# Kernel optimization log

Measured on AMD Instinct MI355X. Metric: run time of the kernel, lower is better.

The kernel has to match this reference:

```python
import jax, jax.numpy as jnp
import numpy as np

B, N, K = 8, 2048, 100  # graphs per batch, nodes per graph, diffpool clusters


def _bn(x, g, b, eps=1e-5):
    # BatchNorm1d in training mode over all B*N nodes (biased variance)
    m = x.mean(axis=(0, 1))
    v = x.var(axis=(0, 1))
    return (x - m) * jax.lax.rsqrt(v + eps) * g + b


def _norm_adj(A):
    # PyG gcn_norm: add remaining self-loops (fill=1), D^-1/2 (A+I) D^-1/2
    n = A.shape[-1]
    d = jnp.diagonal(A, axis1=-2, axis2=-1)
    A_hat = A + jnp.where(d == 0, 1.0, 0.0)[..., :, None] * jnp.eye(n, dtype=A.dtype)
    deg = A_hat.sum(-1)
    dinv = jnp.where(deg > 0, 1.0 / jnp.sqrt(deg), 0.0)
    return dinv[..., :, None] * A_hat * dinv[..., None, :]


def _gcn(An, x, W, b):
    # GCNConv: propagate(x @ W) + bias, with pre-normalized adjacency
    return An @ (x @ W) + b


def _forward(x, adj, W_in, W3030, Wp13, b30, b100, Wfc_pool, bfc_pool,
             W1, b1, W2, b2, gamma30, beta30, gamma100, beta100):
    A_w = _norm_adj(adj)                               # weighted (edge_attr) adjacency
    A_b = _norm_adj((adj > 0).astype(adj.dtype))       # pool convs ignore edge_attr
    # feature branch
    x11 = _bn(_gcn(A_w, x, W_in[0], b30[0]), gamma30[0], beta30[0])
    x12 = _bn(_gcn(A_w, x11, W3030[0], b30[1]), gamma30[1], beta30[1])
    x13 = _bn(_gcn(A_w, x12, W3030[1], b30[2]), gamma30[2], beta30[2])
    x1_out = jnp.concatenate([x11, x12, x13], -1).max(axis=1)   # [B,90]
    # assignment branch
    s11 = _bn(_gcn(A_b, x, W_in[1], b30[3]), gamma30[3], beta30[3])
    s12 = _bn(_gcn(A_b, s11, W3030[2], b30[4]), gamma30[4], beta30[4])
    s13 = _bn(_gcn(A_b, s12, Wp13, b100), gamma100, beta100)
    s1 = jnp.concatenate([s11, s12, s13], -1) @ Wfc_pool + bfc_pool  # [B,N,K]
    # dense_diff_pool (link/entropy losses are unused by the forward output)
    s = jax.nn.softmax(s1, -1)
    p1_x = jnp.einsum('bnk,bnd->bkd', s, x13)          # s^T x  [B,K,30]
    p1_adj = jnp.einsum('bnk,bnl->bkl', s, adj @ s)    # s^T A s  [B,K,K]
    # second stage on pooled (dense, weighted) graph
    A2 = _norm_adj(p1_adj)
    x21 = _bn(_gcn(A2, p1_x, W3030[3], b30[5]), gamma30[5], beta30[5])
    x22 = _bn(_gcn(A2, x21, W3030[4], b30[6]), gamma30[6], beta30[6])
    x23 = _bn(_gcn(A2, x22, W3030[5], b30[7]), gamma30[7], beta30[7])
    x2_out = jnp.concatenate([x21, x22, x23], -1).max(axis=1)   # [B,90]
    h = jnp.concatenate([x1_out, x2_out], -1) @ W1 + b1
    return jax.nn.relu(h) @ W2 + b2                    # [B,6]


def setup_inputs():
    key = jax.random.key(0)
    ks = jax.random.split(key, 12)
    u = jax.random.uniform(ks[0], (B, N, N), dtype=jnp.float32)
    mask = jax.random.uniform(ks[1], (B, N, N)) < 0.05
    A = jnp.triu(u * mask, 1)
    adj = A + jnp.swapaxes(A, -1, -2)
    x = jax.random.normal(ks[2], (B, N, 3), dtype=jnp.float32)
    w = lambda k, s: jax.random.normal(k, s, dtype=jnp.float32) * 0.1
    return dict(
        x=x, adj=adj,
        W_in=w(ks[3], (2, 3, 30)),      # conv11, pool_conv11
        W3030=w(ks[4], (6, 30, 30)),    # conv12, conv13, pool_conv12, conv21..23
        Wp13=w(ks[5], (30, 100)),
        b30=jnp.zeros((8, 30), jnp.float32),
        b100=jnp.zeros((100,), jnp.float32),
        Wfc_pool=w(ks[6], (160, 100)), bfc_pool=jnp.zeros((100,), jnp.float32),
        W1=w(ks[7], (180, 50)), b1=jnp.zeros((50,), jnp.float32),
        W2=w(ks[8], (50, 6)), b2=jnp.zeros((6,), jnp.float32),
        gamma30=jnp.ones((8, 30), jnp.float32), beta30=jnp.zeros((8, 30), jnp.float32),
        gamma100=jnp.ones((100,), jnp.float32), beta100=jnp.zeros((100,), jnp.float32),
    )


def reference(x, adj, W_in, W3030, Wp13, b30, b100, Wfc_pool, bfc_pool,
              W1, b1, W2, b2, gamma30, beta30, gamma100, beta100):
    return _forward(x, adj, W_in, W3030, Wp13, b30, b100, Wfc_pool, bfc_pool,
                    W1, b1, W2, b2, gamma30, beta30, gamma100, beta100)
```

## Files before the change

### kernel.cpp

```cpp
#include <hip/hip_runtime.h>
#include <hip/hip_fp16.h>
#include <cstdint>
#include <cstddef>

#define BATCH 8
#define NN 2048
#define RTOT 16384
#define CAP 176

static constexpr size_t OF_B1W   = 0;
static constexpr size_t OF_B1B   = 3840;
static constexpr size_t OF_B2W   = 7680;
static constexpr size_t OF_B2B   = 11520;
static constexpr size_t OF_B3W   = 15360;
static constexpr size_t OF_B3B   = 15840;
static constexpr size_t OF_S2    = 17440;
static constexpr size_t OF_CNT   = 17620;
static constexpr size_t ZEND     = 17632;
static constexpr size_t OF_ELLV  = 17664;
static constexpr size_t OF_ELLC  = OF_ELLV + 2883584;
static constexpr size_t OF_ROWLEN= OF_ELLC + 1441792;
static constexpr size_t OF_DINVW = OF_ROWLEN + 16384;
static constexpr size_t OF_DINVB = OF_DINVW + 16384;
static constexpr size_t OF_HWB   = OF_DINVB + 16384;
static constexpr size_t OF_HW3   = OF_HWB + 524288;
static constexpr size_t OF_HB100 = OF_HW3 + 262144;
static constexpr size_t OF_ZW    = OF_HB100 + 851968;
static constexpr size_t OF_ZB    = OF_ZW + 524288;
static constexpr size_t OF_X11   = OF_ZB + 1703936;
static constexpr size_t OF_X12   = OF_X11 + 524288;
static constexpr size_t OF_X13   = OF_X12 + 524288;
static constexpr size_t OF_S11   = OF_X13 + 524288;
static constexpr size_t OF_S12   = OF_S11 + 524288;
static constexpr size_t OF_PARTMAX = OF_S12 + 524288;
static constexpr size_t OF_PP    = OF_PARTMAX + 23040;
static constexpr size_t OF_PPOOL = OF_PP + 3328000;

#define FMA4(acc, s, h) { acc.x += (s)*(h).x; acc.y += (s)*(h).y; acc.z += (s)*(h).z; acc.w += (s)*(h).w; }

__device__ __forceinline__ unsigned short f2h(float f) {
  _Float16 h = (_Float16)f;
  return *(unsigned short*)&h;
}
__device__ __forceinline__ float h2f(unsigned short s) {
  _Float16 h = *(_Float16*)&s;
  return (float)h;
}
__device__ __forceinline__ float2 h2f2(unsigned int u) {
  __half2 h = *(__half2*)&u;
  return __half22float2(h);
}

struct __align__(8) us4 { unsigned short x, y, z, w; };

#define ACC8(g, wt) { \
  float2 f0=h2f2((g).x), f1=h2f2((g).y), f2=h2f2((g).z), f3=h2f2((g).w); \
  acc[0] += (wt)*f0.x; acc[1] += (wt)*f0.y; acc[2] += (wt)*f1.x; acc[3] += (wt)*f1.y; \
  acc[4] += (wt)*f2.x; acc[5] += (wt)*f2.y; acc[6] += (wt)*f3.x; acc[7] += (wt)*f3.y; }


__global__ __launch_bounds__(256) void k_build_ell(
    const float* __restrict__ adj, const float* __restrict__ x,
    const float* __restrict__ Win, float* __restrict__ ellv,
    unsigned short* __restrict__ ellc, int* __restrict__ rowlen,
    float* __restrict__ dinvw, float* __restrict__ dinvb,
    unsigned short* __restrict__ Hwb, float* __restrict__ zbase)
{
  int r = blockIdx.x;
  int t = threadIdx.x, lane = t & 63, wv = t >> 6;
  if (blockIdx.x < 69) {
    int zi = blockIdx.x * 256 + t;
    if (zi < (int)ZEND) zbase[zi] = 0.f;
  }
  const float* row = adj + (size_t)r * NN;
  __shared__ int wcnt[4];
  __shared__ float wsumA[4];
  __shared__ float dsh[2];
  float4 a = ((const float4*)row)[t];
  float4 b = ((const float4*)row)[256 + t];
  float vals[8] = {a.x, a.y, a.z, a.w, b.x, b.y, b.z, b.w};
  int cbase0 = t*4, cbase1 = 1024 + t*4;
  int cnt = 0; float sum = 0.f;
#pragma unroll
  for (int k = 0; k < 8; ++k) { sum += vals[k]; cnt += (vals[k] != 0.f) ? 1 : 0; }
  int pre = cnt;
#pragma unroll
  for (int o = 1; o < 64; o <<= 1) { int n = __shfl_up(pre, o); if (lane >= o) pre += n; }
  int excl = pre - cnt;
  int wtot = __shfl(pre, 63);
#pragma unroll
  for (int o = 32; o; o >>= 1) sum += __shfl_down(sum, o);
  if (lane == 0) { wcnt[wv] = wtot; wsumA[wv] = sum; }
  __syncthreads();
  int base = 0;
  for (int w = 0; w < wv; ++w) base += wcnt[w];
  int p = base + excl;
  size_t rb = (size_t)r * CAP;
#pragma unroll
  for (int k = 0; k < 8; ++k) {
    float v = vals[k];
    if (v != 0.f && p < CAP) {
      ellv[rb + p] = v;
      ellc[rb + p] = (unsigned short)((k < 4) ? (cbase0 + k) : (cbase1 + (k - 4)));
      ++p;
    }
  }
  if (t == 0) {
    int tot = wcnt[0] + wcnt[1] + wcnt[2] + wcnt[3];
    float ws = wsumA[0] + wsumA[1] + wsumA[2] + wsumA[3];
    int nnz = tot < CAP ? tot : CAP;
    int n = nnz;
    while ((n & 3) && n < CAP) { ellv[rb + n] = 0.f; ellc[rb + n] = 0; ++n; }
    rowlen[r] = n;
    float dw = rsqrtf(ws + 1.f), db = rsqrtf((float)nnz + 1.f);
    dinvw[r] = dw; dinvb[r] = db;
    dsh[0] = dw; dsh[1] = db;
  }
  __syncthreads();
  if (t < 64) {
    int c = t & 31, side = t >> 5;
    float v = 0.f;
    if (c < 30) {
      float x0 = x[r*3], x1 = x[r*3+1], x2 = x[r*3+2];
      const float* W = Win + side*90;
      v = (x0*W[c] + x1*W[30+c] + x2*W[60+c]) * dsh[side];
    }
    Hwb[(size_t)r*64 + t] = f2h(v);
  }
}

__global__ __launch_bounds__(256) void k_spmm_pair(
    const unsigned short* __restrict__ Hwb, const float* __restrict__ ellv,
    const unsigned short* __restrict__ ellc, const int* __restrict__ rowlen,
    const float* __restrict__ dinvw, const float* __restrict__ dinvb,
    float* __restrict__ Zw, float* __restrict__ Zb,
    float* __restrict__ bktW, float* __restrict__ bktB)
{
  __shared__ float zsW[32][32];
  __shared__ float zsB[32][32];
  int t = threadIdx.x;
  int gid = blockIdx.x * 256 + t;
  int row = gid >> 3, q = gid & 7;
  int side = q >> 2, sub = q & 3;
  int len = rowlen[row];
  const float4* ev = (const float4*)(ellv + (size_t)row * CAP);
  const uint2*  ec = (const uint2*) (ellc + (size_t)row * CAP);
  const uint4* HP = (const uint4*)(Hwb + (size_t)(row >> 11) * (NN*64));
  float acc[8] = {0,0,0,0,0,0,0,0};
  int nit = len >> 2;
  int i = 0;
  for (; i + 2 <= nit; i += 2) {
    float4 v0 = ev[i], v1 = ev[i+1];
    uint2 cc0 = ec[i], cc1 = ec[i+1];
    int a0 = cc0.x & 0xffff, a1 = cc0.x >> 16, a2 = cc0.y & 0xffff, a3 = cc0.y >> 16;
    int e0 = cc1.x & 0xffff, e1 = cc1.x >> 16, e2 = cc1.y & 0xffff, e3 = cc1.y >> 16;
    uint4 g0 = HP[a0*8+q], g1 = HP[a1*8+q], g2 = HP[a2*8+q], g3 = HP[a3*8+q];
    uint4 g4 = HP[e0*8+q], g5 = HP[e1*8+q], g6 = HP[e2*8+q], g7 = HP[e3*8+q];
    float w0 = side ? (v0.x>0.f?1.f:0.f) : v0.x;
    float w1 = side ? (v0.y>0.f?1.f:0.f) : v0.y;
    float w2 = side ? (v0.z>0.f?1.f:0.f) : v0.z;
    float w3 = side ? (v0.w>0.f?1.f:0.f) : v0.w;
    float w4 = side ? (v1.x>0.f?1.f:0.f) : v1.x;
    float w5 = side ? (v1.y>0.f?1.f:0.f) : v1.y;
    float w6 = side ? (v1.z>0.f?1.f:0.f) : v1.z;
    float w7 = side ? (v1.w>0.f?1.f:0.f) : v1.w;
    ACC8(g0, w0); ACC8(g1, w1); ACC8(g2, w2); ACC8(g3, w3);
    ACC8(g4, w4); ACC8(g5, w5); ACC8(g6, w6); ACC8(g7, w7);
  }
  if (i < nit) {
    float4 v = ev[i];
    uint2 cc = ec[i];
    int c0 = cc.x & 0xffff, c1 = cc.x >> 16, c2 = cc.y & 0xffff, c3 = cc.y >> 16;
    uint4 g0 = HP[c0*8+q], g1 = HP[c1*8+q], g2 = HP[c2*8+q], g3 = HP[c3*8+q];
    float w0 = side ? (v.x>0.f?1.f:0.f) : v.x;
    float w1 = side ? (v.y>0.f?1.f:0.f) : v.y;
    float w2 = side ? (v.z>0.f?1.f:0.f) : v.z;
    float w3 = side ? (v.w>0.f?1.f:0.f) : v.w;
    ACC8(g0, w0); ACC8(g1, w1); ACC8(g2, w2); ACC8(g3, w3);
  }
  uint4 hs = HP[(row & (NN-1))*8 + q];
  ACC8(hs, 1.f);
  float d = side ? dinvb[row] : dinvw[row];
#pragma unroll
  for (int k = 0; k < 8; ++k) acc[k] *= d;
  float* Zp = (side ? Zb : Zw) + (size_t)row*32 + sub*8;
  float4 o0 = {acc[0],acc[1],acc[2],acc[3]}, o1 = {acc[4],acc[5],acc[6],acc[7]};
  ((float4*)Zp)[0] = o0; ((float4*)Zp)[1] = o1;
  int rowloc = t >> 3;
  float (*zs)[32] = side ? zsB : zsW;
#pragma unroll
  for (int k = 0; k < 8; ++k) zs[rowloc][sub*8+k] = acc[k];
  __syncthreads();
  int copy = blockIdx.x & 63;
  if (t < 30) {
    float s1 = 0.f, s2 = 0.f;
    for (int r = 0; r < 32; ++r) { float v = zsW[r][t]; s1 += v; s2 += v*v; }
    atomicAdd(&bktW[(t*64+copy)*2],   s1);
    atomicAdd(&bktW[(t*64+copy)*2+1], s2);
  } else if (t >= 64 && t < 94) {
    int c = t - 64;
    float s1 = 0.f, s2 = 0.f;
    for (int r = 0; r < 32; ++r) { float v = zsB[r][c]; s1 += v; s2 += v*v; }
    atomicAdd(&bktB[(c*64+copy)*2],   s1);
    atomicAdd(&bktB[(c*64+copy)*2+1], s2);
  }
}

__global__ __launch_bounds__(256) void k_spmm_l3(
    const unsigned short* __restrict__ Hw3, const unsigned short* __restrict__ Hb100,
    const float* __restrict__ ellv, const unsigned short* __restrict__ ellc,
    const int* __restrict__ rowlen, const float* __restrict__ dinvw,
    const float* __restrict__ dinvb, float* __restrict__ Zw, float* __restrict__ Zb,
    float* __restrict__ bktW3, float* __restrict__ bktB3)
{
  __shared__ float zs[64][32];
  __shared__ float st[200];
  int t = threadIdx.x;
  if (blockIdx.x < 256) {
    int gid = blockIdx.x * 256 + t;
    int row = gid >> 2, q = gid & 3;
    int len = rowlen[row];
    const float4* ev = (const float4*)(ellv + (size_t)row * CAP);
    const uint2*  ec = (const uint2*) (ellc + (size_t)row * CAP);
    const uint4* HP = (const uint4*)(Hw3 + (size_t)(row >> 11) * (NN*32));
    float acc[8] = {0,0,0,0,0,0,0,0};
    int nit = len >> 2;
    int i = 0;
    for (; i + 2 <= nit; i += 2) {
      float4 v0 = ev[i], v1 = ev[i+1];
      uint2 cc0 = ec[i], cc1 = ec[i+1];
      int a0 = cc0.x & 0xffff, a1 = cc0.x >> 16, a2 = cc0.y & 0xffff, a3 = cc0.y >> 16;
      int e0 = cc1.x & 0xffff, e1 = cc1.x >> 16, e2 = cc1.y & 0xffff, e3 = cc1.y >> 16;
      uint4 g0 = HP[a0*4+q], g1 = HP[a1*4+q], g2 = HP[a2*4+q], g3 = HP[a3*4+q];
      uint4 g4 = HP[e0*4+q], g5 = HP[e1*4+q], g6 = HP[e2*4+q], g7 = HP[e3*4+q];
      ACC8(g0, v0.x); ACC8(g1, v0.y); ACC8(g2, v0.z); ACC8(g3, v0.w);
      ACC8(g4, v1.x); ACC8(g5, v1.y); ACC8(g6, v1.z); ACC8(g7, v1.w);
    }
    if (i < nit) {
      float4 v = ev[i];
      uint2 cc = ec[i];
      int c0 = cc.x & 0xffff, c1 = cc.x >> 16, c2 = cc.y & 0xffff, c3 = cc.y >> 16;
      uint4 g0 = HP[c0*4+q], g1 = HP[c1*4+q], g2 = HP[c2*4+q], g3 = HP[c3*4+q];
      ACC8(g0, v.x); ACC8(g1, v.y); ACC8(g2, v.z); ACC8(g3, v.w);
    }
    uint4 hs = HP[(row & (NN-1))*4 + q];
    ACC8(hs, 1.f);
    float d = dinvw[row];
#pragma unroll
    for (int k = 0; k < 8; ++k) acc[k] *= d;
    float* Zp = Zw + (size_t)row*32 + q*8;
    float4 o0 = {acc[0],acc[1],acc[2],acc[3]}, o1 = {acc[4],acc[5],acc[6],acc[7]};
    ((float4*)Zp)[0] = o0; ((float4*)Zp)[1] = o1;
    int rowloc = t >> 2;
#pragma unroll
    for (int k = 0; k < 8; ++k) zs[rowloc][q*8+k] = acc[k];
    __syncthreads();
    if (t < 30) {
      float s1 = 0.f, s2 = 0.f;
      for (int r = 0; r < 64; ++r) { float v = zs[r][t]; s1 += v; s2 += v*v; }
      int copy = blockIdx.x & 7;
      atomicAdd(&bktW3[(t*8+copy)*2],   s1);
      atomicAdd(&bktW3[(t*8+copy)*2+1], s2);
    }
  } else {
    int bid = blockIdx.x - 256;
    for (int i = t; i < 200; i += 256) st[i] = 0.f;
    __syncthreads();
    int gid = bid * 256 + t;
    int row = gid / 13, q = gid - row*13;
    int len = rowlen[row];
    const float4* ev = (const float4*)(ellv + (size_t)row * CAP);
    const uint2*  ec = (const uint2*) (ellc + (size_t)row * CAP);
    const uint4* HP = (const uint4*)(Hb100 + (size_t)(row >> 11) * ((size_t)NN*104));
    float acc[8] = {0,0,0,0,0,0,0,0};
    int nit = len >> 2;
    int i = 0;
    for (; i + 2 <= nit; i += 2) {
      float4 v0 = ev[i], v1 = ev[i+1];
      uint2 cc0 = ec[i], cc1 = ec[i+1];
      int a0 = cc0.x & 0xffff, a1 = cc0.x >> 16, a2 = cc0.y & 0xffff, a3 = cc0.y >> 16;
      int e0 = cc1.x & 0xffff, e1 = cc1.x >> 16, e2 = cc1.y & 0xffff, e3 = cc1.y >> 16;
      uint4 g0 = HP[a0*13+q], g1 = HP[a1*13+q], g2 = HP[a2*13+q], g3 = HP[a3*13+q];
      uint4 g4 = HP[e0*13+q], g5 = HP[e1*13+q], g6 = HP[e2*13+q], g7 = HP[e3*13+q];
      float w0 = (v0.x>0.f?1.f:0.f), w1 = (v0.y>0.f?1.f:0.f);
      float w2 = (v0.z>0.f?1.f:0.f), w3 = (v0.w>0.f?1.f:0.f);
      float w4 = (v1.x>0.f?1.f:0.f), w5 = (v1.y>0.f?1.f:0.f);
      float w6 = (v1.z>0.f?1.f:0.f), w7 = (v1.w>0.f?1.f:0.f);
      ACC8(g0, w0); ACC8(g1, w1); ACC8(g2, w2); ACC8(g3, w3);
      ACC8(g4, w4); ACC8(g5, w5); ACC8(g6, w6); ACC8(g7, w7);
    }
    if (i < nit) {
      float4 v = ev[i];
      uint2 cc = ec[i];
      int c0 = cc.x & 0xffff, c1 = cc.x >> 16, c2 = cc.y & 0xffff, c3 = cc.y >> 16;
      uint4 g0 = HP[c0*13+q], g1 = HP[c1*13+q], g2 = HP[c2*13+q], g3 = HP[c3*13+q];
      float w0 = (v.x>0.f?1.f:0.f), w1 = (v.y>0.f?1.f:0.f);
      float w2 = (v.z>0.f?1.f:0.f), w3 = (v.w>0.f?1.f:0.f);
      ACC8(g0, w0); ACC8(g1, w1); ACC8(g2, w2); ACC8(g3, w3);
    }
    uint4 hs = HP[(row & (NN-1))*13 + q];
    ACC8(hs, 1.f);
    float d = dinvb[row];
#pragma unroll
    for (int k = 0; k < 8; ++k) acc[k] *= d;
    float* Zp = Zb + (size_t)row*104 + q*8;
    float4 o0 = {acc[0],acc[1],acc[2],acc[3]}, o1 = {acc[4],acc[5],acc[6],acc[7]};
    ((float4*)Zp)[0] = o0; ((float4*)Zp)[1] = o1;
    int c0 = q*8;
#pragma unroll
    for (int k = 0; k < 8; ++k) {
      int ch = c0 + k;
      if (ch < 100) { atomicAdd(&st[ch*2], acc[k]); atomicAdd(&st[ch*2+1], acc[k]*acc[k]); }
    }
    __syncthreads();
    int copy = bid & 7;
    for (int i2 = t; i2 < 200; i2 += 256)
      atomicAdd(&bktB3[((i2>>1)*8 + copy)*2 + (i2&1)], st[i2]);
  }
}

template<int LEVEL>
__global__ __launch_bounds__(256) void k_apply_gemm(
    const float* __restrict__ Zw, const float* __restrict__ bktW,
    const float* __restrict__ gW, const float* __restrict__ beW,
    float* __restrict__ xst, const float* __restrict__ Ww,
    const float* __restrict__ dinvw,
    const float* __restrict__ Zb, const float* __restrict__ bktB,
    const float* __restrict__ gB, const float* __restrict__ beB,
    float* __restrict__ sst, const float* __restrict__ Wb,
    const float* __restrict__ dinvb,
    unsigned short* __restrict__ HwOut, unsigned short* __restrict__ HbOut)
{
  constexpr int NGB = (LEVEL == 1) ? 8 : 26;
  constexpr int OSTRIDEB = (LEVEL == 1) ? 32 : 104;
  constexpr int NG = 8 + NGB;
  __shared__ float WwL[30*32];
  __shared__ float WbL[30*OSTRIDEB];
  __shared__ float awL[60], abL[60];
  int t = threadIdx.x;
  if (t < 60) {
    int c = t % 30;
    bool isW = t < 30;
    const float4* p = (const float4*)((isW ? bktW : bktB) + c*128);
    float s1 = 0.f, s2 = 0.f;
#pragma unroll
    for (int k = 0; k < 32; ++k) { float4 v = p[k]; s1 += v.x + v.z; s2 += v.y + v.w; }
    float mean = s1/16384.f, var = s2/16384.f - mean*mean, inv = rsqrtf(var + 1e-5f);
    float aa = (isW ? gW : gB)[c]*inv;
    float* dst = isW ? awL : abL;
    dst[c] = aa; dst[30+c] = (isW ? beW : beB)[c] - mean*aa;
  }
  for (int idx = t; idx < 30*32; idx += 256) {
    int k = idx >> 5, c = idx & 31;
    WwL[idx] = (c < 30) ? Ww[k*30 + c] : 0.f;
  }
  if (LEVEL == 1) {
    for (int idx = t; idx < 30*32; idx += 256) {
      int k = idx >> 5, c = idx & 31;
      WbL[idx] = (c < 30) ? Wb[k*30 + c] : 0.f;
    }
  } else {
    for (int idx = t; idx < 30*OSTRIDEB; idx += 256) {
      int k = idx / OSTRIDEB, j = idx % OSTRIDEB;
      WbL[idx] = (j < 100) ? Wb[k*100 + j] : 0.f;
    }
  }
  __syncthreads();
  int gid = blockIdx.x * 256 + t;
  int row = gid / NG, g = gid % NG;
  if (g < 8) {
    const float4* Z4 = (const float4*)Zw + (size_t)row*8;
    float4 z4[8];
#pragma unroll
    for (int u = 0; u < 8; ++u) z4[u] = Z4[u];
    const float* z = (const float*)z4;
    int ch = 4*g;
    float4 zg = Z4[g];
    float4 xv;
    xv.x = (ch+0 < 30) ? awL[ch+0]*zg.x + awL[30+ch+0] : 0.f;
    xv.y = (ch+1 < 30) ? awL[ch+1]*zg.y + awL[30+ch+1] : 0.f;
    xv.z = (ch+2 < 30) ? awL[ch+2]*zg.z + awL[30+ch+2] : 0.f;
    xv.w = (ch+3 < 30) ? awL[ch+3]*zg.w + awL[30+ch+3] : 0.f;
    ((float4*)xst)[(size_t)row*8+g] = xv;
    float4 o = {0,0,0,0};
#pragma unroll
    for (int k = 0; k < 30; ++k) {
      float xk = awL[k]*z[k] + awL[30+k];
      float4 w = *(const float4*)(WwL + k*32 + 4*g);
      FMA4(o, xk, w);
    }
    float d = dinvw[row];
    us4 pv = { f2h(d*o.x), f2h(d*o.y), f2h(d*o.z), f2h(d*o.w) };
    unsigned short* dst = (LEVEL == 1) ? (HwOut + (size_t)row*64 + 4*g)
                                       : (HwOut + (size_t)row*32 + 4*g);
    *(us4*)dst = pv;
  } else {
    int gb = g - 8;
    const float4* Z4 = (const float4*)Zb + (size_t)row*8;
    float4 z4[8];
#pragma unroll
    for (int u = 0; u < 8; ++u) z4[u] = Z4[u];
    const float* z = (const float*)z4;
    if (gb < 8) {
      int ch = 4*gb;
      float4 zg = Z4[gb];
      float4 sv;
      sv.x = (ch+0 < 30) ? abL[ch+0]*zg.x + abL[30+ch+0] : 0.f;
      sv.y = (ch+1 < 30) ? abL[ch+1]*zg.y + abL[30+ch+1] : 0.f;
      sv.z = (ch+2 < 30) ? abL[ch+2]*zg.z + abL[30+ch+2] : 0.f;
      sv.w = (ch+3 < 30) ? abL[ch+3]*zg.w + abL[30+ch+3] : 0.f;
      ((float4*)sst)[(size_t)row*8+gb] = sv;
    }
    float4 o = {0,0,0,0};
#pragma unroll
    for (int k = 0; k < 30; ++k) {
      float sk = abL[k]*z[k] + abL[30+k];
      float4 w = *(const float4*)(WbL + k*OSTRIDEB + 4*gb);
      FMA4(o, sk, w);
    }
    float d = dinvb[row];
    us4 pv = { f2h(d*o.x), f2h(d*o.y), f2h(d*o.z), f2h(d*o.w) };
    unsigned short* dst = (LEVEL == 1) ? (HbOut + (size_t)row*64 + 32 + 4*gb)
                                       : (HbOut + (size_t)row*104 + 4*gb);
    *(us4*)dst = pv;
  }
}

__global__ __launch_bounds__(256) void k_fcpool(
    const float* __restrict__ Zw3, const float* __restrict__ bktW3,
    const float* __restrict__ gW3, const float* __restrict__ beW3,
    const float* __restrict__ Zb3, const float* __restrict__ bktB3,
    const float* __restrict__ g100, const float* __restrict__ be100,
    const float* __restrict__ s11, const float* __restrict__ s12,
    const float* __restrict__ Wfc, const float* __restrict__ bfc,
    float* __restrict__ x13, unsigned short* __restrict__ S)
{
  __shared__ float shm[14240];
  __shared__ float aw3[60], ab3[200];
  float* feat = shm;
  float* Wl = shm + 10240;
  int t = threadIdx.x;
  int g0 = blockIdx.x * 64;
  if (t < 30) {
    const float4* p = (const float4*)(bktW3 + t*16);
    float s1 = 0.f, s2 = 0.f;
#pragma unroll
    for (int k = 0; k < 4; ++k) { float4 v = p[k]; s1 += v.x + v.z; s2 += v.y + v.w; }
    float mean = s1/16384.f, var = s2/16384.f - mean*mean, inv = rsqrtf(var + 1e-5f);
    float aa = gW3[t]*inv; aw3[t] = aa; aw3[30+t] = beW3[t] - mean*aa;
  } else if (t >= 64 && t < 164) {
    int c = t - 64;
    const float4* p = (const float4*)(bktB3 + c*16);
    float s1 = 0.f, s2 = 0.f;
#pragma unroll
    for (int k = 0; k < 4; ++k) { float4 v = p[k]; s1 += v.x + v.z; s2 += v.y + v.w; }
    float mean = s1/16384.f, var = s2/16384.f - mean*mean, inv = rsqrtf(var + 1e-5f);
    float aa = g100[c]*inv; ab3[c] = aa; ab3[100+c] = be100[c] - mean*aa;
  }
  __syncthreads();
  for (int idx = t; idx < 64*160; idx += 256) {
    int l = idx / 160, c = idx % 160;
    int g = g0 + l;
    float v;
    if (c < 30) v = s11[(size_t)g*32 + c];
    else if (c < 60) v = s12[(size_t)g*32 + (c-30)];
    else { int k = c - 60; v = ab3[k]*Zb3[(size_t)g*104 + k] + ab3[100 + k]; }
    feat[l*160 + c] = v;
  }
  for (int idx = t; idx < 64*32; idx += 256) {
    int l = idx >> 5, c = idx & 31;
    int g = g0 + l;
    x13[(size_t)g*32+c] = (c < 30) ? aw3[c]*Zw3[(size_t)g*32+c] + aw3[30+c] : 0.f;
  }
  int np = t >> 3, kg = t & 7;
  int n0 = np*2, n1 = np*2 + 1;
  int kbase = kg*12 + (kg < 4 ? kg : 4);
  int klen  = kg < 4 ? 13 : 12;
  float a0[13], a1[13];
#pragma unroll
  for (int j = 0; j < 13; ++j) { a0[j] = 0.f; a1[j] = 0.f; }
  for (int ch = 0; ch < 4; ++ch) {
    __syncthreads();
    for (int idx = t; idx < 4000; idx += 256) {
      int r = idx/100, j = idx%100;
      Wl[r*100 + j] = Wfc[(ch*40 + r)*100 + j];
    }
    __syncthreads();
    for (int kk = 0; kk < 40; ++kk) {
      float f0 = feat[n0*160 + ch*40+kk];
      float f1 = feat[n1*160 + ch*40+kk];
#pragma unroll
      for (int j = 0; j < 13; ++j) {
        if (j < klen) {
          float w = Wl[kk*100 + kbase + j];
          a0[j] += f0*w; a1[j] += f1*w;
        }
      }
    }
  }
  __syncthreads();
  float* sRow = shm;
  for (int j = 0; j < klen; ++j) {
    int k = kbase + j;
    sRow[n0*100 + k] = a0[j] + bfc[k];
    sRow[n1*100 + k] = a1[j] + bfc[k];
  }
  __syncthreads();
  int n = t >> 2, part = t & 3;
  int i0 = part*25;
  float m = -3.4e38f;
  for (int i = 0; i < 25; ++i) m = fmaxf(m, sRow[n*100 + i0 + i]);
  m = fmaxf(m, __shfl_xor(m, 1));
  m = fmaxf(m, __shfl_xor(m, 2));
  float ev[25]; float s = 0.f;
  for (int i = 0; i < 25; ++i) { float e = __expf(sRow[n*100 + i0 + i] - m); ev[i] = e; s += e; }
  s += __shfl_xor(s, 1);
  s += __shfl_xor(s, 2);
  float rinv = 1.f / s;
  for (int i = 0; i < 25; ++i) S[(size_t)(g0+n)*104 + i0 + i] = f2h(ev[i] * rinv);
  if (part == 3) {
    S[(size_t)(g0+n)*104 + 100] = 0; S[(size_t)(g0+n)*104 + 101] = 0;
    S[(size_t)(g0+n)*104 + 102] = 0; S[(size_t)(g0+n)*104 + 103] = 0;
  }
}

__global__ __launch_bounds__(256) void k_spmm_as(
    const unsigned short* __restrict__ S, const float* __restrict__ ellv,
    const unsigned short* __restrict__ ellc, const int* __restrict__ rowlen,
    float* __restrict__ Z)
{
  int t = threadIdx.x;
  int gid = blockIdx.x * 256 + t;
  int row = gid / 13, q = gid - row*13;
  int len = rowlen[row];
  const float4* ev = (const float4*)(ellv + (size_t)row * CAP);
  const uint2*  ec = (const uint2*) (ellc + (size_t)row * CAP);
  const uint4* HP = (const uint4*)(S + (size_t)(row >> 11) * ((size_t)NN*104));
  float acc[8] = {0,0,0,0,0,0,0,0};
  int nit = len >> 2;
  int i = 0;
  for (; i + 2 <= nit; i += 2) {
    float4 v0 = ev[i], v1 = ev[i+1];
    uint2 cc0 = ec[i], cc1 = ec[i+1];
    int a0 = cc0.x & 0xffff, a1 = cc0.x >> 16, a2 = cc0.y & 0xffff, a3 = cc0.y >> 16;
    int e0 = cc1.x & 0xffff, e1 = cc1.x >> 16, e2 = cc1.y & 0xffff, e3 = cc1.y >> 16;
    uint4 g0 = HP[a0*13+q], g1 = HP[a1*13+q], g2 = HP[a2*13+q], g3 = HP[a3*13+q];
    uint4 g4 = HP[e0*13+q], g5 = HP[e1*13+q], g6 = HP[e2*13+q], g7 = HP[e3*13+q];
    ACC8(g0, v0.x); ACC8(g1, v0.y); ACC8(g2, v0.z); ACC8(g3, v0.w);
    ACC8(g4, v1.x); ACC8(g5, v1.y); ACC8(g6, v1.z); ACC8(g7, v1.w);
  }
  if (i < nit) {
    float4 v = ev[i];
    uint2 cc = ec[i];
    int c0 = cc.x & 0xffff, c1 = cc.x >> 16, c2 = cc.y & 0xffff, c3 = cc.y >> 16;
    uint4 g0 = HP[c0*13+q], g1 = HP[c1*13+q], g2 = HP[c2*13+q], g3 = HP[c3*13+q];
    ACC8(g0, v.x); ACC8(g1, v.y); ACC8(g2, v.z); ACC8(g3, v.w);
  }
  float* Zp = Z + (size_t)row*104 + q*8;
  float4 o0 = {acc[0],acc[1],acc[2],acc[3]}, o1 = {acc[4],acc[5],acc[6],acc[7]};
  ((float4*)Zp)[0] = o0; ((float4*)Zp)[1] = o1;
}

__global__ __launch_bounds__(256) void k_pool_part(
    const unsigned short* __restrict__ S, const float* __restrict__ x13,
    const float* __restrict__ As, const float* __restrict__ x11,
    const float* __restrict__ x12, float* __restrict__ pp, float* __restrict__ pm)
{
  __shared__ float sL[64][100];
  __shared__ float xL[64][132];
  __shared__ float red[256];
  int t = threadIdx.x;
  int b = blockIdx.x >> 5, chunk = blockIdx.x & 31;
  int g0 = b * 2048 + chunk * 64;
  int kt = t/10, dt = t%10;
  int k0 = kt*4, d0 = dt*13;
  float acc[4][13];
#pragma unroll
  for (int a = 0; a < 4; ++a)
#pragma unroll
    for (int j = 0; j < 13; ++j) acc[a][j] = 0.f;
  for (int idx = t; idx < 64*100; idx += 256) {
    int l = idx/100, k = idx%100;
    sL[l][k] = h2f(S[(size_t)(g0+l)*104 + k]);
  }
  for (int idx = t; idx < 64*130; idx += 256) {
    int l = idx/130, d = idx%130;
    xL[l][d] = d < 30 ? x13[(size_t)(g0+l)*32 + d] : As[(size_t)(g0+l)*104 + (d-30)];
  }
  __syncthreads();
  if (t < 250) {
    for (int kk = 0; kk < 64; ++kk) {
      float sv[4];
#pragma unroll
      for (int a = 0; a < 4; ++a) sv[a] = sL[kk][k0+a];
#pragma unroll
      for (int j = 0; j < 13; ++j) {
        float xv = xL[kk][d0+j];
#pragma unroll
        for (int a = 0; a < 4; ++a) acc[a][j] += sv[a]*xv;
      }
    }
    float* dst = pp + (size_t)blockIdx.x * 13000;
    for (int a = 0; a < 4; ++a)
      for (int j = 0; j < 13; ++j)
        dst[(k0+a)*130 + (d0+j)] = acc[a][j];
  }
  __syncthreads();
  {
    int c = t & 31, rg = t >> 5;
    const float* srcs[3] = {x11, x12, x13};
#pragma unroll
    for (int a = 0; a < 3; ++a) {
      const float* p = srcs[a] + (size_t)(g0+rg)*32 + c;
      float m = -3.4e38f;
#pragma unroll
      for (int it = 0; it < 8; ++it) m = fmaxf(m, p[it*256]);
      red[t] = m;
      __syncthreads();
      if (t < 30) {
        float mm = red[t];
        for (int g = 1; g < 8; ++g) mm = fmaxf(mm, red[g*32+t]);
        pm[(size_t)blockIdx.x*90 + a*30 + t] = mm;
      }
      __syncthreads();
    }
  }
}

__global__ __launch_bounds__(256) void k_pool_reduce(
    const float* __restrict__ pp, float* __restrict__ ppool)
{
  int b = blockIdx.x / 51, blk = blockIdx.x % 51;
  int idx = blk * 256 + threadIdx.x;
  if (idx < 13000) {
    const float* src = pp + (size_t)b * 32 * 13000 + idx;
    float s = 0.f;
#pragma unroll
    for (int c = 0; c < 32; ++c) s += src[c*13000];
    ppool[(size_t)b*13000 + idx] = s;
  }
}

__global__ __launch_bounds__(256) void k_s2fused(
    const float* __restrict__ ppool, const float* __restrict__ partmax,
    const float* __restrict__ Wm,
    const float* __restrict__ g30,
    const float* __restrict__ be30,
    float* __restrict__ bktS2,
    int* __restrict__ cnt,
    const float* __restrict__ W1, const float* __restrict__ b1,
    const float* __restrict__ W2, const float* __restrict__ b2,
    float* __restrict__ out)
{
  __shared__ float A2f[10000];
  __shared__ float buf1[3000];
  __shared__ float buf2[3200];
  __shared__ float WL[960];
  __shared__ float dl[100];
  __shared__ float st1[30], st2[30];
  __shared__ float coef[60];
  __shared__ float x1L[90], x2L[90], hh[50];
  int b = blockIdx.x, t = threadIdx.x;
  for (int idx = t; idx < 13000; idx += 256) {
    float s = ppool[(size_t)b*13000 + idx];
    int k = idx/130, d = idx%130;
    if (d < 30) buf1[k*30 + d] = s;
    else A2f[k*100 + (d-30)] = s;
  }
  __syncthreads();
  if (t < 100 && A2f[t*101] == 0.f) A2f[t*101] = 1.f;
  __syncthreads();
  if (t < 100) {
    float s = 0.f;
    for (int j = 0; j < 100; ++j) s += A2f[t*100 + j];
    dl[t] = s > 0.f ? rsqrtf(s) : 0.f;
  }
  __syncthreads();
  for (int idx = t; idx < 10000; idx += 256) {
    int i = idx/100, j = idx%100;
    A2f[idx] = dl[i]*dl[j]*A2f[idx];
  }
  int rp = t >> 2, cg = t & 3;
  int i0 = rp*2, c0 = cg*8;
  bool act = (t < 200);
  for (int L = 0; L < 3; ++L) {
    if (t < 30) { st1[t] = 0.f; st2[t] = 0.f; }
    const float* W = Wm + L*900;
    for (int idx = t; idx < 960; idx += 256) {
      int k = idx >> 5, c = idx & 31;
      WL[idx] = (c < 30) ? W[k*30 + c] : 0.f;
    }
    __syncthreads();
    if (act) {
      float a0[8] = {0,0,0,0,0,0,0,0}, a1[8] = {0,0,0,0,0,0,0,0};
      for (int k = 0; k < 30; ++k) {
        float xx0 = buf1[i0*30 + k], xx1 = buf1[(i0+1)*30 + k];
        float4 w0 = *(const float4*)&WL[k*32 + c0];
        float4 w1 = *(const float4*)&WL[k*32 + c0 + 4];
        a0[0] += xx0*w0.x; a0[1] += xx0*w0.y; a0[2] += xx0*w0.z; a0[3] += xx0*w0.w;
        a0[4] += xx0*w1.x; a0[5] += xx0*w1.y; a0[6] += xx0*w1.z; a0[7] += xx0*w1.w;
        a1[0] += xx1*w0.x; a1[1] += xx1*w0.y; a1[2] += xx1*w0.z; a1[3] += xx1*w0.w;
        a1[4] += xx1*w1.x; a1[5] += xx1*w1.y; a1[6] += xx1*w1.z; a1[7] += xx1*w1.w;
      }
      float4 s00 = {a0[0],a0[1],a0[2],a0[3]}, s01 = {a0[4],a0[5],a0[6],a0[7]};
      float4 s10 = {a1[0],a1[1],a1[2],a1[3]}, s11v = {a1[4],a1[5],a1[6],a1[7]};
      *(float4*)&buf2[i0*32 + c0]       = s00;
      *(float4*)&buf2[i0*32 + c0 + 4]   = s01;
      *(float4*)&buf2[(i0+1)*32 + c0]   = s10;
      *(float4*)&buf2[(i0+1)*32 + c0+4] = s11v;
    }
    __syncthreads();
    if (act) {
      float z0[8] = {0,0,0,0,0,0,0,0}, z1[8] = {0,0,0,0,0,0,0,0};
      for (int j = 0; j < 100; ++j) {
        float av0 = A2f[i0*100 + j], av1 = A2f[(i0+1)*100 + j];
        float4 t0 = *(const float4*)&buf2[j*32 + c0];
        float4 t1 = *(const float4*)&buf2[j*32 + c0 + 4];
        z0[0] += av0*t0.x; z0[1] += av0*t0.y; z0[2] += av0*t0.z; z0[3] += av0*t0.w;
        z0[4] += av0*t1.x; z0[5] += av0*t1.y; z0[6] += av0*t1.z; z0[7] += av0*t1.w;
        z1[0] += av1*t0.x; z1[1] += av1*t0.y; z1[2] += av1*t0.z; z1[3] += av1*t0.w;
        z1[4] += av1*t1.x; z1[5] += av1*t1.y; z1[6] += av1*t1.z; z1[7] += av1*t1.w;
      }
#pragma unroll
      for (int k = 0; k < 8; ++k) {
        int c = c0 + k;
        if (c < 30) {
          buf1[i0*30 + c]     = z0[k];
          buf1[(i0+1)*30 + c] = z1[k];
          atomicAdd(&st1[c], z0[k] + z1[k]);
          atomicAdd(&st2[c], z0[k]*z0[k] + z1[k]*z1[k]);
        }
      }
    }
    __syncthreads();
    if (t < 30) {
      atomicAdd(&bktS2[(L*30+t)*2],   st1[t]);
      atomicAdd(&bktS2[(L*30+t)*2+1], st2[t]);
    }
    __syncthreads();
    if (t == 0) {
      __threadfence();
      atomicAdd(cnt, 1);
      while (atomicAdd(cnt, 0) < (L+1)*8) {}
      __threadfence();
    }
    __syncthreads();
    if (t < 30) {
      float s1 = atomicAdd(&bktS2[(L*30+t)*2],   0.f);
      float s2 = atomicAdd(&bktS2[(L*30+t)*2+1], 0.f);
      float mean = s1/800.f, var = s2/800.f - mean*mean, inv = rsqrtf(var + 1e-5f);
      float aa = g30[L*30+t]*inv;
      coef[t] = aa; coef[30+t] = be30[L*30+t] - mean*aa;
    }
    __syncthreads();
    if (L < 2) {
      for (int idx = t; idx < 3000; idx += 256) {
        int c = idx % 30;
        buf1[idx] = coef[c]*buf1[idx] + coef[30+c];
      }
      __syncthreads();
      if (t < 30) {
        float m = -3.4e38f;
        for (int i = 0; i < 100; ++i) m = fmaxf(m, buf1[i*30+t]);
        x2L[L*30+t] = m;
      }
      __syncthreads();
    } else {
      if (t < 30) {
        float m = -3.4e38f;
        for (int i = 0; i < 100; ++i) m = fmaxf(m, coef[t]*buf1[i*30+t] + coef[30+t]);
        x2L[60+t] = m;
      }
    }
  }
  if (t < 90) {
    float m = -3.4e38f;
    for (int s = 0; s < 32; ++s) m = fmaxf(m, partmax[(size_t)(b*32+s)*90 + t]);
    x1L[t] = m;
  }
  __syncthreads();
  if (t < 50) {
    float a = b1[t];
    for (int k = 0; k < 90; ++k) a += x1L[k]*W1[k*50+t];
    for (int k = 0; k < 90; ++k) a += x2L[k]*W1[(90+k)*50+t];
    hh[t] = fmaxf(a, 0.f);
  }
  __syncthreads();
  if (t < 6) {
    float a = b2[t];
    for (int j = 0; j < 50; ++j) a += hh[j]*W2[j*6+t];
    out[b*6+t] = a;
  }
}

extern "C" void kernel_launch(void* const* d_in, const int* in_sizes, int n_in,
                              void* d_out, int out_size, void* d_ws, size_t ws_size,
                              hipStream_t stream)
{
  const float* x    = (const float*)d_in[0];
  const float* adj  = (const float*)d_in[1];
  const float* Win  = (const float*)d_in[2];
  const float* W3030= (const float*)d_in[3];
  const float* Wp13 = (const float*)d_in[4];
  const float* Wfc  = (const float*)d_in[7];
  const float* bfc  = (const float*)d_in[8];
  const float* W1   = (const float*)d_in[9];
  const float* b1   = (const float*)d_in[10];
  const float* W2   = (const float*)d_in[11];
  const float* b2   = (const float*)d_in[12];
  const float* g30  = (const float*)d_in[13];
  const float* be30 = (const float*)d_in[14];
  const float* g100 = (const float*)d_in[15];
  const float* be100= (const float*)d_in[16];
  float* out = (float*)d_out;

  float* wsf = (float*)d_ws;
  float* bL1W = wsf + OF_B1W;  float* bL1B = wsf + OF_B1B;
  float* bL2W = wsf + OF_B2W;  float* bL2B = wsf + OF_B2B;
  float* bL3W = wsf + OF_B3W;  float* bL3B = wsf + OF_B3B;
  float* bktS2 = wsf + OF_S2;
  int*   cnt  = (int*)(wsf + OF_CNT);
  float* ellv  = wsf + OF_ELLV;
  unsigned short* ellc = (unsigned short*)(wsf + OF_ELLC);
  int*   rowlen = (int*)(wsf + OF_ROWLEN);
  float* dinvw = wsf + OF_DINVW;
  float* dinvb = wsf + OF_DINVB;
  unsigned short* Hwb   = (unsigned short*)(wsf + OF_HWB);
  unsigned short* Hw3   = (unsigned short*)(wsf + OF_HW3);
  unsigned short* Hb100 = (unsigned short*)(wsf + OF_HB100);
  unsigned short* S     = Hb100;
  float* Zw = wsf + OF_ZW;
  float* Zb = wsf + OF_ZB;
  float* x11 = wsf + OF_X11;
  float* x12 = wsf + OF_X12;
  float* x13 = wsf + OF_X13;
  float* s11 = wsf + OF_S11;
  float* s12 = wsf + OF_S12;
  float* pp  = wsf + OF_PP;
  float* ppool = wsf + OF_PPOOL;
  float* partmax = wsf + OF_PARTMAX;

  k_build_ell<<<RTOT, 256, 0, stream>>>(adj, x, Win, ellv, ellc, rowlen, dinvw, dinvb, Hwb, wsf);

  k_spmm_pair<<<512, 256, 0, stream>>>(Hwb, ellv, ellc, rowlen, dinvw, dinvb, Zw, Zb, bL1W, bL1B);
  k_apply_gemm<1><<<1024, 256, 0, stream>>>(Zw, bL1W, g30+0, be30+0, x11, W3030+0, dinvw,
                                            Zb, bL1B, g30+90, be30+90, s11, W3030+2*900, dinvb, Hwb, Hwb);

  k_spmm_pair<<<512, 256, 0, stream>>>(Hwb, ellv, ellc, rowlen, dinvw, dinvb, Zw, Zb, bL2W, bL2B);
  k_apply_gemm<2><<<2176, 256, 0, stream>>>(Zw, bL2W, g30+30, be30+30, x12, W3030+900, dinvw,
                                            Zb, bL2B, g30+120, be30+120, s12, Wp13, dinvb, Hw3, Hb100);

  k_spmm_l3<<<1088, 256, 0, stream>>>(Hw3, Hb100, ellv, ellc, rowlen, dinvw, dinvb, Zw, Zb, bL3W, bL3B);
  k_fcpool<<<256, 256, 0, stream>>>(Zw, bL3W, g30+60, be30+60, Zb, bL3B, g100, be100,
                                    s11, s12, Wfc, bfc, x13, S);

  k_spmm_as<<<832, 256, 0, stream>>>(S, ellv, ellc, rowlen, Zb );
  k_pool_part<<<256, 256, 0, stream>>>(S, x13, Zb, x11, x12, pp, partmax);
  k_pool_reduce<<<408, 256, 0, stream>>>(pp, ppool);

  k_s2fused<<<BATCH, 256, 0, stream>>>(ppool, partmax, W3030+3*900, g30+150, be30+150,
                                       bktS2, cnt, W1, b1, W2, b2, out);
}
```

Before: 549.0 us.

## Split SpMM row neighbor lists across thread pairs and halve pool chunk size

After: 603.3 us. 1.1x slower.

```diff
diff --git a/kernel.cpp b/kernel.cpp
--- a/kernel.cpp
+++ b/kernel.cpp
@@ -33,8 +33,8 @@
 static constexpr size_t OF_S11   = OF_X13 + 524288;
 static constexpr size_t OF_S12   = OF_S11 + 524288;
 static constexpr size_t OF_PARTMAX = OF_S12 + 524288;
-static constexpr size_t OF_PP    = OF_PARTMAX + 23040;
-static constexpr size_t OF_PPOOL = OF_PP + 3328000;
+static constexpr size_t OF_PP    = OF_PARTMAX + 46080;
+static constexpr size_t OF_PPOOL = OF_PP + 6656000;
 
 #define FMA4(acc, s, h) { acc.x += (s)*(h).x; acc.y += (s)*(h).y; acc.z += (s)*(h).z; acc.w += (s)*(h).w; }
 
@@ -136,11 +136,12 @@
     float* __restrict__ Zw, float* __restrict__ Zb,
     float* __restrict__ bktW, float* __restrict__ bktB)
 {
-  __shared__ float zsW[32][32];
-  __shared__ float zsB[32][32];
+  __shared__ float zsW[16][32];
+  __shared__ float zsB[16][32];
   int t = threadIdx.x;
   int gid = blockIdx.x * 256 + t;
-  int row = gid >> 3, q = gid & 7;
+  int row = gid >> 4, rem = gid & 15;
+  int q = rem >> 1, h = rem & 1;
   int side = q >> 2, sub = q & 3;
   int len = rowlen[row];
   const float4* ev = (const float4*)(ellv + (size_t)row * CAP);
@@ -148,8 +149,10 @@
   const uint4* HP = (const uint4*)(Hwb + (size_t)(row >> 11) * (NN*64));
   float acc[8] = {0,0,0,0,0,0,0,0};
   int nit = len >> 2;
-  int i = 0;
-  for (; i + 2 <= nit; i += 2) {
+  int nh = (nit + 1) >> 1;
+  int i  = h ? nh : 0;
+  int hi = h ? nit : nh;
+  for (; i + 2 <= hi; i += 2) {
     float4 v0 = ev[i], v1 = ev[i+1];
     uint2 cc0 = ec[i], cc1 = ec[i+1];
     int a0 = cc0.x & 0xffff, a1 = cc0.x >> 16, a2 = cc0.y & 0xffff, a3 = cc0.y >> 16;
@@ -167,7 +170,7 @@
     ACC8(g0, w0); ACC8(g1, w1); ACC8(g2, w2); ACC8(g3, w3);
     ACC8(g4, w4); ACC8(g5, w5); ACC8(g6, w6); ACC8(g7, w7);
   }
-  if (i < nit) {
+  if (i < hi) {
     float4 v = ev[i];
     uint2 cc = ec[i];
     int c0 = cc.x & 0xffff, c1 = cc.x >> 16, c2 = cc.y & 0xffff, c3 = cc.y >> 16;
@@ -178,29 +181,35 @@
     float w3 = side ? (v.w>0.f?1.f:0.f) : v.w;
     ACC8(g0, w0); ACC8(g1, w1); ACC8(g2, w2); ACC8(g3, w3);
   }
-  uint4 hs = HP[(row & (NN-1))*8 + q];
-  ACC8(hs, 1.f);
-  float d = side ? dinvb[row] : dinvw[row];
-#pragma unroll
-  for (int k = 0; k < 8; ++k) acc[k] *= d;
-  float* Zp = (side ? Zb : Zw) + (size_t)row*32 + sub*8;
-  float4 o0 = {acc[0],acc[1],acc[2],acc[3]}, o1 = {acc[4],acc[5],acc[6],acc[7]};
-  ((float4*)Zp)[0] = o0; ((float4*)Zp)[1] = o1;
-  int rowloc = t >> 3;
-  float (*zs)[32] = side ? zsB : zsW;
-#pragma unroll
-  for (int k = 0; k < 8; ++k) zs[rowloc][sub*8+k] = acc[k];
+  if (!h) {
+    uint4 hs = HP[(row & (NN-1))*8 + q];
+    ACC8(hs, 1.f);
+  }
+#pragma unroll
+  for (int k = 0; k < 8; ++k) acc[k] += __shfl_xor(acc[k], 1);
+  if (!h) {
+    float d = side ? dinvb[row] : dinvw[row];
+#pragma unroll
+    for (int k = 0; k < 8; ++k) acc[k] *= d;
+    float* Zp = (side ? Zb : Zw) + (size_t)row*32 + sub*8;
+    float4 o0 = {acc[0],acc[1],acc[2],acc[3]}, o1 = {acc[4],acc[5],acc[6],acc[7]};
+    ((float4*)Zp)[0] = o0; ((float4*)Zp)[1] = o1;
+    int rowloc = t >> 4;
+    float (*zs)[32] = side ? zsB : zsW;
+#pragma unroll
+    for (int k = 0; k < 8; ++k) zs[rowloc][sub*8+k] = acc[k];
+  }
   __syncthreads();
   int copy = blockIdx.x & 63;
   if (t < 30) {
     float s1 = 0.f, s2 = 0.f;
-    for (int r = 0; r < 32; ++r) { float v = zsW[r][t]; s1 += v; s2 += v*v; }
+    for (int r = 0; r < 16; ++r) { float v = zsW[r][t]; s1 += v; s2 += v*v; }
     atomicAdd(&bktW[(t*64+copy)*2],   s1);
     atomicAdd(&bktW[(t*64+copy)*2+1], s2);
   } else if (t >= 64 && t < 94) {
     int c = t - 64;
     float s1 = 0.f, s2 = 0.f;
-    for (int r = 0; r < 32; ++r) { float v = zsB[r][c]; s1 += v; s2 += v*v; }
+    for (int r = 0; r < 16; ++r) { float v = zsB[r][c]; s1 += v; s2 += v*v; }
     atomicAdd(&bktB[(c*64+copy)*2],   s1);
     atomicAdd(&bktB[(c*64+copy)*2+1], s2);
   }
@@ -213,20 +222,23 @@
     const float* __restrict__ dinvb, float* __restrict__ Zw, float* __restrict__ Zb,
     float* __restrict__ bktW3, float* __restrict__ bktB3)
 {
-  __shared__ float zs[64][32];
+  __shared__ float zs[32][32];
   __shared__ float st[200];
   int t = threadIdx.x;
-  if (blockIdx.x < 256) {
+  if (blockIdx.x < 512) {
     int gid = blockIdx.x * 256 + t;
-    int row = gid >> 2, q = gid & 3;
+    int row = gid >> 3, rem = gid & 7;
+    int q = rem >> 1, h = rem & 1;
     int len = rowlen[row];
     const float4* ev = (const float4*)(ellv + (size_t)row * CAP);
     const uint2*  ec = (const uint2*) (ellc + (size_t)row * CAP);
     const uint4* HP = (const uint4*)(Hw3 + (size_t)(row >> 11) * (NN*32));
     float acc[8] = {0,0,0,0,0,0,0,0};
     int nit = len >> 2;
-    int i = 0;
-    for (; i + 2 <= nit; i += 2) {
+    int nh = (nit + 1) >> 1;
+    int i  = h ? nh : 0;
+    int hi = h ? nit : nh;
+    for (; i + 2 <= hi; i += 2) {
       float4 v0 = ev[i], v1 = ev[i+1];
       uint2 cc0 = ec[i], cc1 = ec[i+1];
       int a0 = cc0.x & 0xffff, a1 = cc0.x >> 16, a2 = cc0.y & 0xffff, a3 = cc0.y >> 16;
@@ -236,46 +248,55 @@
       ACC8(g0, v0.x); ACC8(g1, v0.y); ACC8(g2, v0.z); ACC8(g3, v0.w);
       ACC8(g4, v1.x); ACC8(g5, v1.y); ACC8(g6, v1.z); ACC8(g7, v1.w);
     }
-    if (i < nit) {
+    if (i < hi) {
       float4 v = ev[i];
       uint2 cc = ec[i];
       int c0 = cc.x & 0xffff, c1 = cc.x >> 16, c2 = cc.y & 0xffff, c3 = cc.y >> 16;
       uint4 g0 = HP[c0*4+q], g1 = HP[c1*4+q], g2 = HP[c2*4+q], g3 = HP[c3*4+q];
       ACC8(g0, v.x); ACC8(g1, v.y); ACC8(g2, v.z); ACC8(g3, v.w);
     }
-    uint4 hs = HP[(row & (NN-1))*4 + q];
-    ACC8(hs, 1.f);
-    float d = dinvw[row];
-#pragma unroll
-    for (int k = 0; k < 8; ++k) acc[k] *= d;
-    float* Zp = Zw + (size_t)row*32 + q*8;
-    float4 o0 = {acc[0],acc[1],acc[2],acc[3]}, o1 = {acc[4],acc[5],acc[6],acc[7]};
-    ((float4*)Zp)[0] = o0; ((float4*)Zp)[1] = o1;
-    int rowloc = t >> 2;
-#pragma unroll
-    for (int k = 0; k < 8; ++k) zs[rowloc][q*8+k] = acc[k];
+    if (!h) {
+      uint4 hs = HP[(row & (NN-1))*4 + q];
+      ACC8(hs, 1.f);
+    }
+#pragma unroll
+    for (int k = 0; k < 8; ++k) acc[k] += __shfl_xor(acc[k], 1);
+    if (!h) {
+      float d = dinvw[row];
+#pragma unroll
+      for (int k = 0; k < 8; ++k) acc[k] *= d;
+      float* Zp = Zw + (size_t)row*32 + q*8;
+      float4 o0 = {acc[0],acc[1],acc[2],acc[3]}, o1 = {acc[4],acc[5],acc[6],acc[7]};
+      ((float4*)Zp)[0] = o0; ((float4*)Zp)[1] = o1;
+      int rowloc = t >> 3;
+#pragma unroll
+      for (int k = 0; k < 8; ++k) zs[rowloc][q*8+k] = acc[k];
+    }
     __syncthreads();
     if (t < 30) {
       float s1 = 0.f, s2 = 0.f;
-      for (int r = 0; r < 64; ++r) { float v = zs[r][t]; s1 += v; s2 += v*v; }
+      for (int r = 0; r < 32; ++r) { float v = zs[r][t]; s1 += v; s2 += v*v; }
       int copy = blockIdx.x & 7;
       atomicAdd(&bktW3[(t*8+copy)*2],   s1);
       atomicAdd(&bktW3[(t*8+copy)*2+1], s2);
     }
   } else {
-    int bid = blockIdx.x - 256;
+    int bid = blockIdx.x - 512;
     for (int i = t; i < 200; i += 256) st[i] = 0.f;
     __syncthreads();
     int gid = bid * 256 + t;
-    int row = gid / 13, q = gid - row*13;
+    int row = gid / 26, rem = gid - row*26;
+    int q = rem >> 1, h = rem & 1;
     int len = rowlen[row];
     const float4* ev = (const float4*)(ellv + (size_t)row * CAP);
     const uint2*  ec = (const uint2*) (ellc + (size_t)row * CAP);
     const uint4* HP = (const uint4*)(Hb100 + (size_t)(row >> 11) * ((size_t)NN*104));
     float acc[8] = {0,0,0,0,0,0,0,0};
     int nit = len >> 2;
-    int i = 0;
-    for (; i + 2 <= nit; i += 2) {
+    int nh = (nit + 1) >> 1;
+    int i  = h ? nh : 0;
+    int hi = h ? nit : nh;
+    for (; i + 2 <= hi; i += 2) {
       float4 v0 = ev[i], v1 = ev[i+1];
       uint2 cc0 = ec[i], cc1 = ec[i+1];
       int a0 = cc0.x & 0xffff, a1 = cc0.x >> 16, a2 = cc0.y & 0xffff, a3 = cc0.y >> 16;
@@ -289,7 +310,7 @@
       ACC8(g0, w0); ACC8(g1, w1); ACC8(g2, w2); ACC8(g3, w3);
       ACC8(g4, w4); ACC8(g5, w5); ACC8(g6, w6); ACC8(g7, w7);
     }
-    if (i < nit) {
+    if (i < hi) {
       float4 v = ev[i];
       uint2 cc = ec[i];
       int c0 = cc.x & 0xffff, c1 = cc.x >> 16, c2 = cc.y & 0xffff, c3 = cc.y >> 16;
@@ -298,19 +319,25 @@
       float w2 = (v.z>0.f?1.f:0.f), w3 = (v.w>0.f?1.f:0.f);
       ACC8(g0, w0); ACC8(g1, w1); ACC8(g2, w2); ACC8(g3, w3);
     }
-    uint4 hs = HP[(row & (NN-1))*13 + q];
-    ACC8(hs, 1.f);
-    float d = dinvb[row];
-#pragma unroll
-    for (int k = 0; k < 8; ++k) acc[k] *= d;
-    float* Zp = Zb + (size_t)row*104 + q*8;
-    float4 o0 = {acc[0],acc[1],acc[2],acc[3]}, o1 = {acc[4],acc[5],acc[6],acc[7]};
-    ((float4*)Zp)[0] = o0; ((float4*)Zp)[1] = o1;
-    int c0 = q*8;
-#pragma unroll
-    for (int k = 0; k < 8; ++k) {
-      int ch = c0 + k;
-      if (ch < 100) { atomicAdd(&st[ch*2], acc[k]); atomicAdd(&st[ch*2+1], acc[k]*acc[k]); }
+    if (!h) {
+      uint4 hs = HP[(row & (NN-1))*13 + q];
+      ACC8(hs, 1.f);
+    }
+#pragma unroll
+    for (int k = 0; k < 8; ++k) acc[k] += __shfl_xor(acc[k], 1);
+    if (!h) {
+      float d = dinvb[row];
+#pragma unroll
+      for (int k = 0; k < 8; ++k) acc[k] *= d;
+      float* Zp = Zb + (size_t)row*104 + q*8;
+      float4 o0 = {acc[0],acc[1],acc[2],acc[3]}, o1 = {acc[4],acc[5],acc[6],acc[7]};
+      ((float4*)Zp)[0] = o0; ((float4*)Zp)[1] = o1;
+      int c0 = q*8;
+#pragma unroll
+      for (int k = 0; k < 8; ++k) {
+        int ch = c0 + k;
+        if (ch < 100) { atomicAdd(&st[ch*2], acc[k]); atomicAdd(&st[ch*2+1], acc[k]*acc[k]); }
+      }
     }
     __syncthreads();
     int copy = bid & 7;
@@ -531,15 +558,18 @@
 {
   int t = threadIdx.x;
   int gid = blockIdx.x * 256 + t;
-  int row = gid / 13, q = gid - row*13;
+  int row = gid / 26, rem = gid - row*26;
+  int q = rem >> 1, h = rem & 1;
   int len = rowlen[row];
   const float4* ev = (const float4*)(ellv + (size_t)row * CAP);
   const uint2*  ec = (const uint2*) (ellc + (size_t)row * CAP);
   const uint4* HP = (const uint4*)(S + (size_t)(row >> 11) * ((size_t)NN*104));
   float acc[8] = {0,0,0,0,0,0,0,0};
   int nit = len >> 2;
-  int i = 0;
-  for (; i + 2 <= nit; i += 2) {
+  int nh = (nit + 1) >> 1;
+  int i  = h ? nh : 0;
+  int hi = h ? nit : nh;
+  for (; i + 2 <= hi; i += 2) {
     float4 v0 = ev[i], v1 = ev[i+1];
     uint2 cc0 = ec[i], cc1 = ec[i+1];
     int a0 = cc0.x & 0xffff, a1 = cc0.x >> 16, a2 = cc0.y & 0xffff, a3 = cc0.y >> 16;
@@ -549,16 +579,20 @@
     ACC8(g0, v0.x); ACC8(g1, v0.y); ACC8(g2, v0.z); ACC8(g3, v0.w);
     ACC8(g4, v1.x); ACC8(g5, v1.y); ACC8(g6, v1.z); ACC8(g7, v1.w);
   }
-  if (i < nit) {
+  if (i < hi) {
     float4 v = ev[i];
     uint2 cc = ec[i];
     int c0 = cc.x & 0xffff, c1 = cc.x >> 16, c2 = cc.y & 0xffff, c3 = cc.y >> 16;
     uint4 g0 = HP[c0*13+q], g1 = HP[c1*13+q], g2 = HP[c2*13+q], g3 = HP[c3*13+q];
     ACC8(g0, v.x); ACC8(g1, v.y); ACC8(g2, v.z); ACC8(g3, v.w);
   }
-  float* Zp = Z + (size_t)row*104 + q*8;
-  float4 o0 = {acc[0],acc[1],acc[2],acc[3]}, o1 = {acc[4],acc[5],acc[6],acc[7]};
-  ((float4*)Zp)[0] = o0; ((float4*)Zp)[1] = o1;
+#pragma unroll
+  for (int k = 0; k < 8; ++k) acc[k] += __shfl_xor(acc[k], 1);
+  if (!h) {
+    float* Zp = Z + (size_t)row*104 + q*8;
+    float4 o0 = {acc[0],acc[1],acc[2],acc[3]}, o1 = {acc[4],acc[5],acc[6],acc[7]};
+    ((float4*)Zp)[0] = o0; ((float4*)Zp)[1] = o1;
+  }
 }
 
 __global__ __launch_bounds__(256) void k_pool_part(
@@ -566,12 +600,12 @@
     const float* __restrict__ As, const float* __restrict__ x11,
     const float* __restrict__ x12, float* __restrict__ pp, float* __restrict__ pm)
 {
-  __shared__ float sL[64][100];
-  __shared__ float xL[64][132];
+  __shared__ float sL[32][100];
+  __shared__ float xL[32][132];
   __shared__ float red[256];
   int t = threadIdx.x;
-  int b = blockIdx.x >> 5, chunk = blockIdx.x & 31;
-  int g0 = b * 2048 + chunk * 64;
+  int b = blockIdx.x >> 6, chunk = blockIdx.x & 63;
+  int g0 = b * 2048 + chunk * 32;
   int kt = t/10, dt = t%10;
   int k0 = kt*4, d0 = dt*13;
   float acc[4][13];
@@ -579,17 +613,17 @@
   for (int a = 0; a < 4; ++a)
 #pragma unroll
     for (int j = 0; j < 13; ++j) acc[a][j] = 0.f;
-  for (int idx = t; idx < 64*100; idx += 256) {
+  for (int idx = t; idx < 32*100; idx += 256) {
     int l = idx/100, k = idx%100;
     sL[l][k] = h2f(S[(size_t)(g0+l)*104 + k]);
   }
-  for (int idx = t; idx < 64*130; idx += 256) {
+  for (int idx = t; idx < 32*130; idx += 256) {
     int l = idx/130, d = idx%130;
     xL[l][d] = d < 30 ? x13[(size_t)(g0+l)*32 + d] : As[(size_t)(g0+l)*104 + (d-30)];
   }
   __syncthreads();
   if (t < 250) {
-    for (int kk = 0; kk < 64; ++kk) {
+    for (int kk = 0; kk < 32; ++kk) {
       float sv[4];
 #pragma unroll
       for (int a = 0; a < 4; ++a) sv[a] = sL[kk][k0+a];
@@ -614,7 +648,7 @@
       const float* p = srcs[a] + (size_t)(g0+rg)*32 + c;
       float m = -3.4e38f;
 #pragma unroll
-      for (int it = 0; it < 8; ++it) m = fmaxf(m, p[it*256]);
+      for (int it = 0; it < 4; ++it) m = fmaxf(m, p[it*256]);
       red[t] = m;
       __syncthreads();
       if (t < 30) {
@@ -633,10 +667,10 @@
   int b = blockIdx.x / 51, blk = blockIdx.x % 51;
   int idx = blk * 256 + threadIdx.x;
   if (idx < 13000) {
-    const float* src = pp + (size_t)b * 32 * 13000 + idx;
+    const float* src = pp + (size_t)b * 64 * 13000 + idx;
     float s = 0.f;
 #pragma unroll
-    for (int c = 0; c < 32; ++c) s += src[c*13000];
+    for (int c = 0; c < 64; ++c) s += src[c*13000];
     ppool[(size_t)b*13000 + idx] = s;
   }
 }
@@ -775,7 +809,7 @@
   }
   if (t < 90) {
     float m = -3.4e38f;
-    for (int s = 0; s < 32; ++s) m = fmaxf(m, partmax[(size_t)(b*32+s)*90 + t]);
+    for (int s = 0; s < 64; ++s) m = fmaxf(m, partmax[(size_t)(b*64+s)*90 + t]);
     x1L[t] = m;
   }
   __syncthreads();
@@ -842,20 +876,20 @@
 
   k_build_ell<<<RTOT, 256, 0, stream>>>(adj, x, Win, ellv, ellc, rowlen, dinvw, dinvb, Hwb, wsf);
 
-  k_spmm_pair<<<512, 256, 0, stream>>>(Hwb, ellv, ellc, rowlen, dinvw, dinvb, Zw, Zb, bL1W, bL1B);
+  k_spmm_pair<<<1024, 256, 0, stream>>>(Hwb, ellv, ellc, rowlen, dinvw, dinvb, Zw, Zb, bL1W, bL1B);
   k_apply_gemm<1><<<1024, 256, 0, stream>>>(Zw, bL1W, g30+0, be30+0, x11, W3030+0, dinvw,
                                             Zb, bL1B, g30+90, be30+90, s11, W3030+2*900, dinvb, Hwb, Hwb);
 
-  k_spmm_pair<<<512, 256, 0, stream>>>(Hwb, ellv, ellc, rowlen, dinvw, dinvb, Zw, Zb, bL2W, bL2B);
+  k_spmm_pair<<<1024, 256, 0, stream>>>(Hwb, ellv, ellc, rowlen, dinvw, dinvb, Zw, Zb, bL2W, bL2B);
   k_apply_gemm<2><<<2176, 256, 0, stream>>>(Zw, bL2W, g30+30, be30+30, x12, W3030+900, dinvw,
                                             Zb, bL2B, g30+120, be30+120, s12, Wp13, dinvb, Hw3, Hb100);
 
-  k_spmm_l3<<<1088, 256, 0, stream>>>(Hw3, Hb100, ellv, ellc, rowlen, dinvw, dinvb, Zw, Zb, bL3W, bL3B);
+  k_spmm_l3<<<2176, 256, 0, stream>>>(Hw3, Hb100, ellv, ellc, rowlen, dinvw, dinvb, Zw, Zb, bL3W, bL3B);
   k_fcpool<<<256, 256, 0, stream>>>(Zw, bL3W, g30+60, be30+60, Zb, bL3B, g100, be100,
                                     s11, s12, Wfc, bfc, x13, S);
 
-  k_spmm_as<<<832, 256, 0, stream>>>(S, ellv, ellc, rowlen, Zb );
-  k_pool_part<<<256, 256, 0, stream>>>(S, x13, Zb, x11, x12, pp, partmax);
+  k_spmm_as<<<1664, 256, 0, stream>>>(S, ellv, ellc, rowlen, Zb );
+  k_pool_part<<<512, 256, 0, stream>>>(S, x13, Zb, x11, x12, pp, partmax);
   k_pool_reduce<<<408, 256, 0, stream>>>(pp, ppool);
 
   k_s2fused<<<BATCH, 256, 0, stream>>>(ppool, partmax, W3030+3*900, g30+150, be30+150,
```
